# Kernel tuning notes

Measured on AMD Instinct MI355X. Metric: run time of the kernel, lower is better.

Reference implementation:

```python
import jax, jax.numpy as jnp
import numpy as np


@jax.custom_vjp
def spike(mem, v_th):
    # Heaviside forward, triangular surrogate backward (gamma=1.0)
    return (mem >= v_th).astype(mem.dtype)


def _spike_fwd(mem, v_th):
    return spike(mem, v_th), (mem, v_th)


def _spike_bwd(res, g):
    mem, v_th = res
    surr = jnp.clip(1.0 - jnp.abs(mem - v_th), 0.0)  # gamma = 1
    return (g * surr, jnp.zeros_like(v_th))  # torch returns None for threshold grad


spike.defvjp(_spike_fwd, _spike_bwd)


def setup_inputs() -> dict:
    key = jax.random.key(0)
    ks = jax.random.split(key, 6)
    T, B, C, H, W = 8, 16, 256, 32, 32
    NH, HID = 4, 64
    x = jax.random.normal(ks[0], (T, B, C, H, W), dtype=jnp.float32)
    decay_param = jnp.float32(np.log(0.85 / 0.15))  # logit(0.85)
    v_th = jnp.float32(0.5)
    W1 = jax.random.normal(ks[1], (NH, HID, T), dtype=jnp.float32) * 0.1
    b1 = jax.random.normal(ks[2], (NH, HID), dtype=jnp.float32) * 0.01
    W2 = jax.random.normal(ks[3], (NH, T, HID), dtype=jnp.float32) * 0.1
    b2 = jax.random.normal(ks[4], (NH, T), dtype=jnp.float32) * 0.01
    att_w = jnp.ones((NH,), dtype=jnp.float32) / NH
    return {"x": x, "decay_param": decay_param, "v_th": v_th,
            "W1": W1, "b1": b1, "W2": W2, "b2": b2, "att_w": att_w}


def reference(x, decay_param, v_th, W1, b1, W2, b2, att_w):
    T, B, C, H, W = x.shape
    d = jax.nn.sigmoid(decay_param)

    def step(carry, inp):
        mem, spk = carry  # detached states, as in the torch module
        m = d * (mem - v_th * spk) + inp
        denom = jnp.mean(jnp.abs(m), axis=(1, 2, 3), keepdims=True) + 1e-6
        m = m / denom
        s = spike(m, v_th)
        carry = (jax.lax.stop_gradient(m), jax.lax.stop_gradient(s))
        return carry, s

    init = (jnp.zeros_like(x[0]), jnp.zeros_like(x[0]))
    _, spikes = jax.lax.scan(step, init, x)          # [T,B,C,H,W]

    feats = spikes.reshape(T, B, C * H * W)          # [T,B,F]
    summary = feats.mean(axis=2).T                   # [B,T]
    # multi-head MLP attention over time
    h = jax.nn.relu(jnp.einsum('bt,nht->bnh', summary, W1) + b1[None])  # [B,NH,HID]
    maps = jnp.einsum('bnh,nth->bnt', h, W2) + b2[None]                  # [B,NH,T]
    weighted = jnp.sum(maps * att_w[None, :, None], axis=1)              # [B,T]
    aw = jax.nn.softmax(weighted, axis=-1).T[:, :, None]                 # [T,B,1]
    out = jnp.sum(feats * aw, axis=0)                                    # [B,F]
    return out
```

## Files before the change

### kernel.cpp

```cpp
#include <hip/hip_runtime.h>

#define NT    8
#define NB    16
#define FS    262144
#define TPB   256
#define BPB   32
#define GRID  (NB*BPB)
#define CHK   8
#define ELB   (TPB*CHK*4)
#define SPIN_CAP (1L<<26)

#define WS_NEED 50688

__global__ __launch_bounds__(TPB, 2)
void bispike_kernel(const float* __restrict__ x,
                    const float* __restrict__ decay_p,
                    const float* __restrict__ vth_p,
                    const float* __restrict__ W1,
                    const float* __restrict__ b1,
                    const float* __restrict__ W2,
                    const float* __restrict__ b2,
                    const float* __restrict__ att_w,
                    float* __restrict__ out,
                    double* __restrict__ bsum,
                    double* __restrict__ dbc,
                    int* __restrict__ cnt,
                    int* __restrict__ cbc)
{
    const int tid  = threadIdx.x;
    const int lane = tid & 63;
    const int wid  = tid >> 6;
    const int b    = blockIdx.x % NB;
    const int bg   = blockIdx.x / NB;
    const bool leader = (bg == 0);

    const double dec  = 1.0 / (1.0 + exp(-(double)decay_p[0]));
    const double vth  = (double)vth_p[0];
    const double csub = dec * vth;

    double   u[CHK * 4];
    float4   xv[CHK];
    unsigned sm[NT];

    {
        const float* p = x + (size_t)b * FS + (size_t)bg * ELB + tid * 4;
        #pragma unroll
        for (int k = 0; k < CHK; ++k) xv[k] = *(const float4*)(p + k * (TPB * 4));
    }
    double lsum;
    {
        double n0 = 0.0, n1 = 0.0, n2 = 0.0, n3 = 0.0;
        #pragma unroll
        for (int k = 0; k < CHK; ++k) {
            u[k*4+0] = (double)xv[k].x; n0 += fabs(u[k*4+0]);
            u[k*4+1] = (double)xv[k].y; n1 += fabs(u[k*4+1]);
            u[k*4+2] = (double)xv[k].z; n2 += fabs(u[k*4+2]);
            u[k*4+3] = (double)xv[k].w; n3 += fabs(u[k*4+3]);
        }
        lsum = (n0 + n1) + (n2 + n3);
    }

    __shared__ double dred[4];
    __shared__ double denom_s;

    #pragma unroll 1
    for (int t = 0; t < NT; ++t) {
        if (t < NT - 1) {
            const float* p = x + ((size_t)(t + 1) * NB + b) * FS
                               + (size_t)bg * ELB + tid * 4;
            #pragma unroll
            for (int k = 0; k < CHK; ++k) xv[k] = *(const float4*)(p + k * (TPB * 4));
        }

        double ls = lsum;
        #pragma unroll
        for (int off = 32; off > 0; off >>= 1)
            ls += __shfl_down(ls, off, 64);
        if (lane == 0) dred[wid] = ls;
        __syncthreads();

        if (tid < 64) {
            const double bs = (dred[0] + dred[1]) + (dred[2] + dred[3]);
            double* slot = bsum + (size_t)(t * NB + b) * BPB;
            if (!leader) {
                if (lane == 0) {
                    __hip_atomic_store(slot + bg, -bs, __ATOMIC_RELAXED,
                                       __HIP_MEMORY_SCOPE_AGENT);
                    double dv; long it = 0;
                    for (;;) {
                        dv = __hip_atomic_load(&dbc[t * NB + b], __ATOMIC_RELAXED,
                                               __HIP_MEMORY_SCOPE_AGENT);
                        if (__double_as_longlong(dv) != 0) break;
                        if (++it > SPIN_CAP) break;
                        __builtin_amdgcn_s_sleep(8);
                    }
                    denom_s = dv;
                }
            } else {
                const bool act = (lane >= 1 && lane < 32);
                double v = 0.0; long it = 0;
                for (;;) {
                    if (act)
                        v = __hip_atomic_load(slot + lane, __ATOMIC_RELAXED,
                                              __HIP_MEMORY_SCOPE_AGENT);
                    if (__all(!act || __double_as_longlong(v) != 0)) break;
                    if (++it > SPIN_CAP) break;
                    __builtin_amdgcn_s_sleep(2);
                }
                double tot = (lane == 0) ? bs : ((lane < 32) ? -v : 0.0);
                #pragma unroll
                for (int off = 32; off > 0; off >>= 1)
                    tot += __shfl_down(tot, off, 64);
                if (lane == 0) {
                    const double dn = tot / (double)FS + 1e-6;
                    __hip_atomic_store(&dbc[t * NB + b], dn, __ATOMIC_RELAXED,
                                       __HIP_MEMORY_SCOPE_AGENT);
                    denom_s = dn;
                }
            }
        }
        __syncthreads();
        const double denom = denom_s;

        const double thr = vth * denom;
        const double a   = dec * (1.0 / denom);
        unsigned smt = 0;
        if (t < NT - 1) {
            double n0 = 0.0, n1 = 0.0, n2 = 0.0, n3 = 0.0;
            #pragma unroll
            for (int k = 0; k < CHK; ++k) {
                const double xn0 = (double)xv[k].x, xn1 = (double)xv[k].y,
                             xn2 = (double)xv[k].z, xn3 = (double)xv[k].w;
                double un;
                bool s0 = (u[k*4+0] >= thr); if (s0) smt |= 1u << (k*4+0);
                un = fma(a, u[k*4+0], xn0); if (s0) un -= csub;
                u[k*4+0] = un; n0 += fabs(un);
                bool s1 = (u[k*4+1] >= thr); if (s1) smt |= 1u << (k*4+1);
                un = fma(a, u[k*4+1], xn1); if (s1) un -= csub;
                u[k*4+1] = un; n1 += fabs(un);
                bool s2 = (u[k*4+2] >= thr); if (s2) smt |= 1u << (k*4+2);
                un = fma(a, u[k*4+2], xn2); if (s2) un -= csub;
                u[k*4+2] = un; n2 += fabs(un);
                bool s3 = (u[k*4+3] >= thr); if (s3) smt |= 1u << (k*4+3);
                un = fma(a, u[k*4+3], xn3); if (s3) un -= csub;
                u[k*4+3] = un; n3 += fabs(un);
            }
            lsum = (n0 + n1) + (n2 + n3);
        } else {
            #pragma unroll
            for (int j = 0; j < CHK * 4; ++j)
                if (u[j] >= thr) smt |= 1u << j;
        }
        sm[t] = smt;
    }

    __shared__ int ired[NT][4];
    #pragma unroll
    for (int t = 0; t < NT; ++t) {
        int c = __popc(sm[t]);
        #pragma unroll
        for (int off = 32; off > 0; off >>= 1)
            c += __shfl_down(c, off, 64);
        if (lane == 0) ired[t][wid] = c;
    }
    __syncthreads();

    __shared__ double summ_s[NT];
    __shared__ int totc_s[NT];

    if (tid < 64) {
        int* cb = cnt + b * (NT * BPB);
        if (!leader) {
            if (lane < NT) {
                int tot = (ired[lane][0] + ired[lane][1])
                        + (ired[lane][2] + ired[lane][3]);
                __hip_atomic_store(cb + lane * BPB + bg, tot + 1,
                                   __ATOMIC_RELAXED, __HIP_MEMORY_SCOPE_AGENT);
            }
            const bool act = (lane < NT);
            int cv = 0; long it = 0;
            for (;;) {
                if (act)
                    cv = __hip_atomic_load(&cbc[b * NT + lane], __ATOMIC_RELAXED,
                                           __HIP_MEMORY_SCOPE_AGENT);
                if (__all(!act || cv != 0)) break;
                if (++it > SPIN_CAP) break;
                __builtin_amdgcn_s_sleep(8);
            }
            if (act) totc_s[lane] = cv - 1;
        } else {
            const bool act = (lane >= 1 && lane < 32);
            int vt[NT]; long it = 0;
            for (;;) {
                bool ok = true;
                #pragma unroll
                for (int t = 0; t < NT; ++t) {
                    if (act) {
                        vt[t] = __hip_atomic_load(cb + t * BPB + lane,
                                                  __ATOMIC_RELAXED,
                                                  __HIP_MEMORY_SCOPE_AGENT);
                        ok = ok && (vt[t] > 0);
                    }
                }
                if (__all(ok)) break;
                if (++it > SPIN_CAP) break;
                __builtin_amdgcn_s_sleep(2);
            }
            #pragma unroll
            for (int t = 0; t < NT; ++t) {
                int s;
                if (lane == 0)      s = (ired[t][0] + ired[t][1])
                                      + (ired[t][2] + ired[t][3]);
                else if (act)       s = vt[t] - 1;
                else                s = 0;
                #pragma unroll
                for (int off = 32; off > 0; off >>= 1)
                    s += __shfl_down(s, off, 64);
                if (lane == 0) {
                    totc_s[t] = s;
                    __hip_atomic_store(&cbc[b * NT + t], s + 1,
                                       __ATOMIC_RELAXED, __HIP_MEMORY_SCOPE_AGENT);
                }
            }
        }
    }
    __syncthreads();
    if (tid < NT)
        summ_s[tid] = (double)totc_s[tid] / (double)FS;
    __syncthreads();

    __shared__ double h_s[4 * 64];
    __shared__ double wmat_s[NT];
    {
        int nh = tid >> 6, hd = tid & 63;
        double acc = 0.0;
        #pragma unroll
        for (int t = 0; t < NT; ++t)
            acc += summ_s[t] * (double)W1[nh * 512 + hd * 8 + t];
        acc += (double)b1[nh * 64 + hd];
        h_s[tid] = fmax(acc, 0.0);
    }
    __syncthreads();
    if (tid < NT) {
        double w = 0.0;
        for (int nh = 0; nh < 4; ++nh) {
            double macc = 0.0;
            for (int hd = 0; hd < 64; ++hd)
                macc += h_s[nh * 64 + hd] * (double)W2[nh * 512 + tid * 64 + hd];
            macc += (double)b2[nh * 8 + tid];
            w += macc * (double)att_w[nh];
        }
        wmat_s[tid] = w;
    }
    __syncthreads();

    double awr[NT];
    {
        double mx = wmat_s[0];
        #pragma unroll
        for (int t = 1; t < NT; ++t) mx = fmax(mx, wmat_s[t]);
        double ss = 0.0;
        #pragma unroll
        for (int t = 0; t < NT; ++t) { awr[t] = exp(wmat_s[t] - mx); ss += awr[t]; }
        #pragma unroll
        for (int t = 0; t < NT; ++t) awr[t] = awr[t] / ss;
    }

    float* po = out + (size_t)b * FS + (size_t)bg * ELB + tid * 4;
    #pragma unroll
    for (int k = 0; k < CHK; ++k) {
        double o[4] = {0.0, 0.0, 0.0, 0.0};
        #pragma unroll
        for (int t = 0; t < NT; ++t) {
            const unsigned smt = sm[t];
            o[0] += ((smt >> (k * 4 + 0)) & 1) ? awr[t] : 0.0;
            o[1] += ((smt >> (k * 4 + 1)) & 1) ? awr[t] : 0.0;
            o[2] += ((smt >> (k * 4 + 2)) & 1) ? awr[t] : 0.0;
            o[3] += ((smt >> (k * 4 + 3)) & 1) ? awr[t] : 0.0;
        }
        *(float4*)(po + k * (TPB * 4)) =
            make_float4((float)o[0], (float)o[1], (float)o[2], (float)o[3]);
    }
}

__global__ void diag_kernel(float* out, int code) {
    out[0] = 100000.0f + (float)code;
}

extern "C" void kernel_launch(void* const* d_in, const int* in_sizes, int n_in,
                              void* d_out, int out_size, void* d_ws, size_t ws_size,
                              hipStream_t stream) {
    const float* x     = (const float*)d_in[0];
    const float* decay = (const float*)d_in[1];
    const float* vth   = (const float*)d_in[2];
    const float* W1    = (const float*)d_in[3];
    const float* b1    = (const float*)d_in[4];
    const float* W2    = (const float*)d_in[5];
    const float* b2    = (const float*)d_in[6];
    const float* att   = (const float*)d_in[7];
    float* out = (float*)d_out;

    if (ws_size < WS_NEED) {
        diag_kernel<<<1, 1, 0, stream>>>(out, 999);
        return;
    }

    double* bsum = (double*)d_ws;
    double* dbc  = (double*)((char*)d_ws + 32768);
    int*    cnt  = (int*)((char*)d_ws + 33792);
    int*    cbc  = (int*)((char*)d_ws + 50176);

    hipMemsetAsync(d_ws, 0, WS_NEED, stream);

    hipGetLastError();
    bispike_kernel<<<dim3(GRID), dim3(TPB), 0, stream>>>(
        x, decay, vth, W1, b1, W2, b2, att, out, bsum, dbc, cnt, cbc);
    hipError_t err = hipGetLastError();
    if (err != hipSuccess) {
        diag_kernel<<<1, 1, 0, stream>>>(out, (int)err);
    }
}
```

Baseline: 235.1 us.

## Double blocks per batch, halve per-thread chunk, reuse sync buffers for counts

Doubles the number of blocks per batch sample (1024 total) while halving each thread's element chunk, and raises launch bounds to 4 blocks per CU so every block stays co-resident with higher occupancy. Wave 0 now issues its next-timestep prefetch only after the cross-block denominator handshake, while the other waves prefetch early. The spike-count exchange reuses the bsum/dbc slots, with negative values marking the second phase, instead of separate int arrays, and spin sleeps are shortened. The risks are more leader polling per handshake (63 slots) and reliance on all 1024 blocks being resident, which the spin-wait barriers require to avoid hanging.

```diff
diff --git a/kernel.cpp b/kernel.cpp
--- a/kernel.cpp
+++ b/kernel.cpp
@@ -4,15 +4,15 @@
 #define NB    16
 #define FS    262144
 #define TPB   256
-#define BPB   32
+#define BPB   64
 #define GRID  (NB*BPB)
-#define CHK   8
+#define CHK   4
 #define ELB   (TPB*CHK*4)
 #define SPIN_CAP (1L<<26)
 
-#define WS_NEED 50688
-
-__global__ __launch_bounds__(TPB, 2)
+#define WS_NEED 66560
+
+__global__ __launch_bounds__(TPB, 4)
 void bispike_kernel(const float* __restrict__ x,
                     const float* __restrict__ decay_p,
                     const float* __restrict__ vth_p,
@@ -23,15 +23,13 @@
                     const float* __restrict__ att_w,
                     float* __restrict__ out,
                     double* __restrict__ bsum,
-                    double* __restrict__ dbc,
-                    int* __restrict__ cnt,
-                    int* __restrict__ cbc)
+                    double* __restrict__ dbc)
 {
     const int tid  = threadIdx.x;
     const int lane = tid & 63;
     const int wid  = tid >> 6;
-    const int b    = blockIdx.x % NB;
-    const int bg   = blockIdx.x / NB;
+    const int b    = blockIdx.x & 15;
+    const int bg   = blockIdx.x >> 4;
     const bool leader = (bg == 0);
 
     const double dec  = 1.0 / (1.0 + exp(-(double)decay_p[0]));
@@ -65,7 +63,7 @@
 
     #pragma unroll 1
     for (int t = 0; t < NT; ++t) {
-        if (t < NT - 1) {
+        if (wid != 0 && t < NT - 1) {
             const float* p = x + ((size_t)(t + 1) * NB + b) * FS
                                + (size_t)bg * ELB + tid * 4;
             #pragma unroll
@@ -92,12 +90,12 @@
                                                __HIP_MEMORY_SCOPE_AGENT);
                         if (__double_as_longlong(dv) != 0) break;
                         if (++it > SPIN_CAP) break;
-                        __builtin_amdgcn_s_sleep(8);
+                        __builtin_amdgcn_s_sleep(4);
                     }
                     denom_s = dv;
                 }
             } else {
-                const bool act = (lane >= 1 && lane < 32);
+                const bool act = (lane >= 1);
                 double v = 0.0; long it = 0;
                 for (;;) {
                     if (act)
@@ -105,9 +103,9 @@
                                               __HIP_MEMORY_SCOPE_AGENT);
                     if (__all(!act || __double_as_longlong(v) != 0)) break;
                     if (++it > SPIN_CAP) break;
-                    __builtin_amdgcn_s_sleep(2);
-                }
-                double tot = (lane == 0) ? bs : ((lane < 32) ? -v : 0.0);
+                    __builtin_amdgcn_s_sleep(1);
+                }
+                double tot = (lane == 0) ? bs : -v;
                 #pragma unroll
                 for (int off = 32; off > 0; off >>= 1)
                     tot += __shfl_down(tot, off, 64);
@@ -117,6 +115,13 @@
                                        __HIP_MEMORY_SCOPE_AGENT);
                     denom_s = dn;
                 }
+            }
+            if (t < NT - 1) {
+                const float* p = x + ((size_t)(t + 1) * NB + b) * FS
+                                   + (size_t)bg * ELB + tid * 4;
+                #pragma unroll
+                for (int k = 0; k < CHK; ++k)
+                    xv[k] = *(const float4*)(p + k * (TPB * 4));
             }
         }
         __syncthreads();
@@ -165,60 +170,52 @@
     }
     __syncthreads();
 
+    __shared__ int totc_s[NT];
     __shared__ double summ_s[NT];
-    __shared__ int totc_s[NT];
 
     if (tid < 64) {
-        int* cb = cnt + b * (NT * BPB);
         if (!leader) {
             if (lane < NT) {
                 int tot = (ired[lane][0] + ired[lane][1])
                         + (ired[lane][2] + ired[lane][3]);
-                __hip_atomic_store(cb + lane * BPB + bg, tot + 1,
-                                   __ATOMIC_RELAXED, __HIP_MEMORY_SCOPE_AGENT);
+                __hip_atomic_store(&bsum[(size_t)(lane * NB + b) * BPB + bg],
+                                   (double)(tot + 1), __ATOMIC_RELAXED,
+                                   __HIP_MEMORY_SCOPE_AGENT);
             }
             const bool act = (lane < NT);
-            int cv = 0; long it = 0;
+            double cv = 1.0; long it = 0;
             for (;;) {
                 if (act)
-                    cv = __hip_atomic_load(&cbc[b * NT + lane], __ATOMIC_RELAXED,
+                    cv = __hip_atomic_load(&dbc[lane * NB + b], __ATOMIC_RELAXED,
                                            __HIP_MEMORY_SCOPE_AGENT);
-                if (__all(!act || cv != 0)) break;
+                if (__all(!act || cv < 0.0)) break;
                 if (++it > SPIN_CAP) break;
-                __builtin_amdgcn_s_sleep(8);
-            }
-            if (act) totc_s[lane] = cv - 1;
+                __builtin_amdgcn_s_sleep(4);
+            }
+            if (act) totc_s[lane] = (int)(-cv) - 1;
         } else {
-            const bool act = (lane >= 1 && lane < 32);
-            int vt[NT]; long it = 0;
-            for (;;) {
-                bool ok = true;
-                #pragma unroll
-                for (int t = 0; t < NT; ++t) {
-                    if (act) {
-                        vt[t] = __hip_atomic_load(cb + t * BPB + lane,
-                                                  __ATOMIC_RELAXED,
-                                                  __HIP_MEMORY_SCOPE_AGENT);
-                        ok = ok && (vt[t] > 0);
-                    }
-                }
-                if (__all(ok)) break;
-                if (++it > SPIN_CAP) break;
-                __builtin_amdgcn_s_sleep(2);
-            }
-            #pragma unroll
+            #pragma unroll 1
             for (int t = 0; t < NT; ++t) {
-                int s;
-                if (lane == 0)      s = (ired[t][0] + ired[t][1])
-                                      + (ired[t][2] + ired[t][3]);
-                else if (act)       s = vt[t] - 1;
-                else                s = 0;
+                const bool act = (lane >= 1);
+                double v = 0.0; long it = 0;
+                for (;;) {
+                    if (act)
+                        v = __hip_atomic_load(
+                                &bsum[(size_t)(t * NB + b) * BPB + lane],
+                                __ATOMIC_RELAXED, __HIP_MEMORY_SCOPE_AGENT);
+                    if (__all(!act || v > 0.0)) break;
+                    if (++it > SPIN_CAP) break;
+                    __builtin_amdgcn_s_sleep(1);
+                }
+                int s = (lane == 0)
+                          ? (ired[t][0] + ired[t][1]) + (ired[t][2] + ired[t][3])
+                          : (int)v - 1;
                 #pragma unroll
                 for (int off = 32; off > 0; off >>= 1)
                     s += __shfl_down(s, off, 64);
                 if (lane == 0) {
                     totc_s[t] = s;
-                    __hip_atomic_store(&cbc[b * NT + t], s + 1,
+                    __hip_atomic_store(&dbc[t * NB + b], -(double)(s + 1),
                                        __ATOMIC_RELAXED, __HIP_MEMORY_SCOPE_AGENT);
                 }
             }
@@ -306,15 +303,13 @@
     }
 
     double* bsum = (double*)d_ws;
-    double* dbc  = (double*)((char*)d_ws + 32768);
-    int*    cnt  = (int*)((char*)d_ws + 33792);
-    int*    cbc  = (int*)((char*)d_ws + 50176);
+    double* dbc  = (double*)((char*)d_ws + 65536);
 
     hipMemsetAsync(d_ws, 0, WS_NEED, stream);
 
     hipGetLastError();
     bispike_kernel<<<dim3(GRID), dim3(TPB), 0, stream>>>(
-        x, decay, vth, W1, b1, W2, b2, att, out, bsum, dbc, cnt, cbc);
+        x, decay, vth, W1, b1, W2, b2, att, out, bsum, dbc);
     hipError_t err = hipGetLastError();
     if (err != hipSuccess) {
         diag_kernel<<<1, 1, 0, stream>>>(out, (int)err);
```

Result: no change. 233.0 us (-0.9%).
